# Optimization experiments

Measured on AMD Instinct MI355X. Metric: run time of the kernel, lower is better.

The kernel has to match this reference:

```python
import jax, jax.numpy as jnp
import numpy as np

GRAPH = 50  # top-k neighbors


def setup_inputs() -> dict:
    key = jax.random.key(0)
    k1, k2, k3, k4, k5 = jax.random.split(key, 5)
    B, N, D, C = 2048, 50000, 256, 100
    return {
        "features": jax.random.normal(k1, (B, D), dtype=jnp.float32),
        "anchor_feature": jax.random.normal(k2, (N, D), dtype=jnp.float32),
        "labels": jax.random.randint(k3, (B,), 0, C),
        "t_labels": jax.random.randint(k4, (B,), 0, C),
        "anchor_label": jax.random.randint(k5, (N,), 0, C),
    }


def reference(features, anchor_feature, labels, t_labels, anchor_label):
    # mode == 'knn_sim', reduction=False; t_labels is unpacked but unused.
    # [B, N] dot-product similarity
    sim = jnp.matmul(features, anchor_feature.T)
    # top-k values and indices along anchor dim
    topk_vals, topk_idx = jax.lax.top_k(sim, GRAPH)  # [B, k]
    # label-match mask gathered at the top-k anchors (equivalent to
    # building the full [B, N] eq-mask then torch.gather along dim 1,
    # but gathers anchor labels first to avoid the dense mask)
    nn_labels = anchor_label[topk_idx]               # [B, k]
    mask_k = (labels[:, None] == nn_labels).astype(jnp.float32)
    mean_log_prob_pos = mask_k.sum(axis=1) / GRAPH   # [B]
    mean_sim = topk_vals.sum(axis=1) / GRAPH         # [B]
    # NaN scrub (x != x) -> 0, as in the torch code
    mean_log_prob_pos = jnp.where(jnp.isnan(mean_log_prob_pos), 0.0, mean_log_prob_pos)
    loss = -mean_log_prob_pos                        # [B] (reduction=False)
    return loss, mean_sim
```

## Files before the change

### kernel.cpp

```cpp
#include <hip/hip_runtime.h>
#include <math.h>

#define B_ROWS 2048
#define N_ANCH 50000
#define DIM    256
#define TOPK   50

#define BT 128
#define AT 256
#define KC 32
#define NCHUNK 8
#define NCH 16
#define CHUNK 3125
#define NTILES 13
#define NSAMP 4096
#define CAPG 2048

#define NRB (B_ROWS / BT)
#define TSF (NRB * 8 * 512)
#define TSA (NCH * NTILES * 8 * 1024)

typedef __attribute__((ext_vector_type(8))) short bf16x8;
typedef __attribute__((ext_vector_type(8))) unsigned short u16x8;
typedef __attribute__((ext_vector_type(4))) float f32x4;

#define OFF_B 0
#define OFF_A 16384
#define BUFB  24576
#define SMEM_S (3 * BUFB)
#define SMEM_L (2 * BUFB)

__device__ __forceinline__ void gl_lds16(const void* g, void* l) {
    __builtin_amdgcn_global_load_lds(
        (const __attribute__((address_space(1))) unsigned int*)g,
        (__attribute__((address_space(3))) unsigned int*)l, 16, 0, 0);
}

template<int N>
__device__ __forceinline__ void wait_vmcnt() {
    asm volatile("s_waitcnt vmcnt(%0)" :: "n"(N) : "memory");
}
__device__ __forceinline__ void wait_lgkm0() {
    asm volatile("s_waitcnt lgkmcnt(0)" ::: "memory");
}
__device__ __forceinline__ void pipe_bar() {
    asm volatile("" ::: "memory");
    __builtin_amdgcn_s_barrier();
    asm volatile("" ::: "memory");
}

__device__ __forceinline__ unsigned short f2bf(float x) {
    unsigned u = __float_as_uint(x);
    u += 0x7FFFu + ((u >> 16) & 1u);
    return (unsigned short)(u >> 16);
}

__device__ __forceinline__ unsigned f2ord(float f) {
    unsigned u = __float_as_uint(f);
    return (u & 0x80000000u) ? ~u : (u | 0x80000000u);
}
__device__ __forceinline__ float ord2f(unsigned o) {
    return (o & 0x80000000u) ? __uint_as_float(o & 0x7FFFFFFFu) : __uint_as_float(~o);
}


__global__ __launch_bounds__(256)
void fnorm_feat(const float* __restrict__ x, float* __restrict__ fnorm)
{
    const int lane = threadIdx.x & 63, w = threadIdx.x >> 6;
    const int row  = blockIdx.x * 4 + w;
    float4 v = ((const float4*)(x + (size_t)row * DIM))[lane];
    float s = v.x * v.x + v.y * v.y + v.z * v.z + v.w * v.w;
    #pragma unroll
    for (int off = 32; off; off >>= 1) s += __shfl_down(s, off);
    if (lane == 0) fnorm[row] = sqrtf(s);
}

__global__ __launch_bounds__(256)
void amax_anc(const float* __restrict__ x, int nrows, unsigned* __restrict__ outbits)
{
    __shared__ float wmax[4];
    const int lane = threadIdx.x & 63, w = threadIdx.x >> 6;
    float mx = 0.f;
    for (int i = 0; i < 32; ++i) {
        const int row = blockIdx.x * 128 + w * 32 + i;
        if (row < nrows) {
            float4 v = ((const float4*)(x + (size_t)row * DIM))[lane];
            float s = v.x * v.x + v.y * v.y + v.z * v.z + v.w * v.w;
            #pragma unroll
            for (int off = 32; off; off >>= 1) s += __shfl_down(s, off);
            mx = fmaxf(mx, s);
        }
    }
    if (lane == 0) wmax[w] = mx;
    __syncthreads();
    if (threadIdx.x == 0) {
        float m = fmaxf(fmaxf(wmax[0], wmax[1]), fmaxf(wmax[2], wmax[3]));
        atomicMax(outbits, __float_as_uint(m));
    }
}

__device__ __forceinline__ u16x8 cvt8h(const float4 v0, const float4 v1) {
    float f[8] = {v0.x, v0.y, v0.z, v0.w, v1.x, v1.y, v1.z, v1.w};
    u16x8 h;
    #pragma unroll
    for (int j = 0; j < 8; ++j) h[j] = f2bf(f[j]);
    return h;
}

__global__ __launch_bounds__(256)
void split_pack_feat(const float* __restrict__ x, unsigned short* __restrict__ hi)
{
    const int S  = blockIdx.x * 256 + threadIdx.x;
    const int s  = S & 511;
    const int c  = (S >> 9) & 7;
    const int rb = S >> 12;
    const int r  = s & 127;
    const int kq = s >> 7;
    const int row = (rb << 7) + r;
    const int k   = (c << 5) + (kq << 3);
    const float4* src = (const float4*)(x + (size_t)row * DIM + k);
    *(u16x8*)(hi + (size_t)S * 8) = cvt8h(src[0], src[1]);
}

__global__ __launch_bounds__(256)
void split_pack_anc(const float* __restrict__ x, unsigned short* __restrict__ hi)
{
    const int S    = blockIdx.x * 256 + threadIdx.x;
    const int s    = S & 1023;
    const int c    = (S >> 10) & 7;
    const int tg   = S >> 13;
    const int cidx = tg / NTILES;
    const int tile = tg - cidx * NTILES;
    int a = cidx * CHUNK + (tile << 8) + (s & 255);
    if (a >= N_ANCH) a = N_ANCH - 1;
    const int k = (c << 5) + ((s >> 8) << 3);
    const float4* src = (const float4*)(x + (size_t)a * DIM + k);
    *(u16x8*)(hi + (size_t)S * 8) = cvt8h(src[0], src[1]);
}

#define STAGE_LOADS 3
__device__ __forceinline__ void stage_tile(unsigned char* sb,
                                           const unsigned short* __restrict__ Bsrc,
                                           const unsigned short* __restrict__ Asrc,
                                           int w, int lane)
{
    #pragma unroll
    for (int i = 0; i < 2; ++i) {
        const int t = (w << 1) + i;
        gl_lds16(Bsrc + ((size_t)t << 9) + (lane << 3), sb + OFF_B + (t << 10));
    }
    gl_lds16(Asrc + (((w << 6) + lane) << 3), sb + OFF_A + (w << 10));
}

__device__ __forceinline__ void compute_tile(const unsigned char* sb,
                                             int wm, int wn, int quad, int lx,
                                             f32x4 (&acc)[4][4])
{
    bf16x8 bf[4], af[4];
    #pragma unroll
    for (int tn = 0; tn < 4; ++tn) {
        const int a = (wn << 6) + (tn << 4) + lx;
        bf[tn] = *(const bf16x8*)(sb + OFF_B + (quad << 12) + (a << 4));
    }
    #pragma unroll
    for (int tm = 0; tm < 4; ++tm) {
        const int r = (wm << 6) + (tm << 4) + lx;
        af[tm] = *(const bf16x8*)(sb + OFF_A + (quad << 11) + (r << 4));
    }
    __builtin_amdgcn_s_setprio(1);
    #pragma unroll
    for (int tm = 0; tm < 4; ++tm)
        #pragma unroll
        for (int tn = 0; tn < 4; ++tn)
            acc[tm][tn] = __builtin_amdgcn_mfma_f32_16x16x32_bf16(af[tm], bf[tn], acc[tm][tn], 0, 0, 0);
    __builtin_amdgcn_s_setprio(0);
}

__global__ __launch_bounds__(512, 4)
void knn_sample_gemm(const unsigned short* __restrict__ pfhi,
                     const unsigned short* __restrict__ pahi,
                     float* __restrict__ sims)
{
    __shared__ __align__(16) unsigned char sMem[SMEM_S];

    const int tid  = threadIdx.x;
    const int w    = tid >> 6;
    const int lane = tid & 63;
    const int quad = lane >> 4;
    const int lx   = lane & 15;
    const int wm   = w >> 2;
    const int wn   = w & 3;

    const int id   = blockIdx.x;
    const int xcd  = id & 7;
    const int t    = id >> 3;
    const int rb   = t & 15;
    const int cidx = ((t >> 4) << 3) | xcd;
    const int rbase = rb * BT;
    const int tg    = cidx * NTILES;

    auto bsrc = [&](int c) { return pahi + (((size_t)(tg << 3)) + c) * 8192; };
    auto asrc = [&](int c) { return pfhi + (((size_t)(rb << 3)) + c) * 4096; };

    f32x4 acc[4][4];
    const f32x4 z = {0.f, 0.f, 0.f, 0.f};
    #pragma unroll
    for (int tm = 0; tm < 4; ++tm)
        #pragma unroll
        for (int tn = 0; tn < 4; ++tn) acc[tm][tn] = z;

    stage_tile(sMem + 0 * BUFB, bsrc(0), asrc(0), w, lane);
    stage_tile(sMem + 1 * BUFB, bsrc(1), asrc(1), w, lane);
    __syncthreads();

    for (int it = 0; it < NCHUNK; ++it) {
        if (it + 2 < NCHUNK)
            stage_tile(sMem + ((it + 2) % 3) * BUFB, bsrc(it + 2), asrc(it + 2), w, lane);
        compute_tile(sMem + (it % 3) * BUFB, wm, wn, quad, lx, acc);
        wait_lgkm0();
        if (it + 2 < NCHUNK)      wait_vmcnt<STAGE_LOADS>();
        else if (it + 1 < NCHUNK) wait_vmcnt<0>();
        pipe_bar();
    }

    #pragma unroll
    for (int tm = 0; tm < 4; ++tm)
        #pragma unroll
        for (int tn = 0; tn < 4; ++tn)
            #pragma unroll
            for (int reg = 0; reg < 4; ++reg) {
                int row = rbase + (wm << 6) + (tm << 4) + (quad << 2) + reg;
                int col = (wn << 6) + (tn << 4) + lx;
                sims[(size_t)row * NSAMP + cidx * AT + col] = acc[tm][tn][reg];
            }
}

__global__ __launch_bounds__(256)
void bisect_thresh(const float* __restrict__ sims,
                   uint2* __restrict__ cand, int* __restrict__ cnt,
                   float* __restrict__ Tcut, float* __restrict__ eps2arr,
                   const float* __restrict__ fnorm, const unsigned* __restrict__ amaxb)
{
    __shared__ float sv[NSAMP];
    __shared__ float s_rmin[4], s_rmax[4];
    __shared__ int   s_c, s_ns;

    const int row = blockIdx.x;
    const int tid = threadIdx.x;
    const int lane = tid & 63, w = tid >> 6;
    const unsigned long long below = (lane == 0) ? 0ull : (~0ull >> (64 - lane));

    const float anorm = sqrtf(__uint_as_float(*amaxb));
    const float eps2  = 2.f * (0.004f * fnorm[row] * anorm + 0.1f);

    const float4* S4 = (const float4*)(sims + (size_t)row * NSAMP);
    for (int i = tid; i < NSAMP / 4; i += 256) ((float4*)sv)[i] = S4[i];
    __syncthreads();

    float lmin = INFINITY, lmax = -INFINITY;
    for (int e0 = 0; e0 < NSAMP; e0 += 256) {
        float v = sv[e0 + tid];
        lmin = fminf(lmin, v); lmax = fmaxf(lmax, v);
    }
    #pragma unroll
    for (int off = 32; off; off >>= 1) {
        lmin = fminf(lmin, __shfl_down(lmin, off));
        lmax = fmaxf(lmax, __shfl_down(lmax, off));
    }
    if (lane == 0) { s_rmin[w] = lmin; s_rmax[w] = lmax; }
    __syncthreads();
    float lo = fminf(fminf(s_rmin[0], s_rmin[1]), fminf(s_rmin[2], s_rmin[3]));
    float mx = fmaxf(fmaxf(s_rmax[0], s_rmax[1]), fmaxf(s_rmax[2], s_rmax[3]));
    float hi = ord2f(f2ord(mx) + 1);
    int clo = NSAMP;
    for (int it = 0; it < 32 && clo > 64; ++it) {
        float mid = 0.5f * (lo + hi);
        if (tid == 0) s_c = 0;
        __syncthreads();
        int lc = 0;
        for (int e0 = 0; e0 < NSAMP; e0 += 256) lc += (sv[e0 + tid] >= mid);
        #pragma unroll
        for (int off = 32; off; off >>= 1) lc += __shfl_down(lc, off);
        if (lane == 0) atomicAdd(&s_c, lc);
        __syncthreads();
        int c = s_c;
        if (c >= TOPK) { lo = mid; clo = c; } else hi = mid;
        __syncthreads();
    }
    const float cut = lo - eps2;
    if (tid == 0) { Tcut[row] = cut; eps2arr[row] = eps2; s_ns = 0; }
    __syncthreads();

    for (int e0 = 0; e0 < NSAMP; e0 += 256) {
        int e = e0 + tid;
        float v = sv[e];
        bool pred = (v >= cut);
        unsigned long long mk = __ballot(pred);
        int base = 0;
        if (lane == 0) base = atomicAdd(&s_ns, __popcll(mk));
        base = __shfl(base, 0);
        if (pred) {
            int ofs = base + __popcll(mk & below);
            int anchor = (e >> 8) * CHUNK + (e & 255);
            if (ofs < CAPG)
                cand[(size_t)row * CAPG + ofs] = make_uint2(__float_as_uint(v), (unsigned)anchor);
        }
    }
    __syncthreads();
    if (tid == 0) cnt[row] = s_ns;
}

__global__ __launch_bounds__(512, 4)
void knn_mfma_append(const unsigned short* __restrict__ pfhi,
                     const unsigned short* __restrict__ pahi,
                     const float* __restrict__ Tcut,
                     uint2* __restrict__ cand, int* __restrict__ cnt)
{
    __shared__ __align__(16) unsigned char sMem[SMEM_L];
    __shared__ float s_T[BT];

    const int tid  = threadIdx.x;
    const int w    = tid >> 6;
    const int lane = tid & 63;
    const int quad = lane >> 4;
    const int lx   = lane & 15;
    const int wm   = w >> 2;
    const int wn   = w & 3;

    const int id   = blockIdx.x;
    const int xcd  = id & 7;
    const int t    = id >> 3;
    const int rb   = t & 15;
    const int gseq = t >> 4;
    const int g    = (gseq << 3) | xcd;
    const int cidx = g & 15;
    const int tile = 1 + (g >> 4);
    const int rbase = rb * BT;

    if (tid < BT) s_T[tid] = Tcut[rbase + tid];

    auto bsrc = [&](int c) {
        return pahi + (((size_t)((cidx * NTILES + tile) << 3)) + c) * 8192;
    };
    auto asrc = [&](int c) { return pfhi + (((size_t)(rb << 3)) + c) * 4096; };

    stage_tile(sMem, bsrc(0), asrc(0), w, lane);
    __syncthreads();

    float thr[4][4];
    #pragma unroll
    for (int tm = 0; tm < 4; ++tm)
        #pragma unroll
        for (int reg = 0; reg < 4; ++reg)
            thr[tm][reg] = s_T[(wm << 6) + (tm << 4) + (quad << 2) + reg];

    f32x4 acc[4][4];
    const f32x4 z = {0.f, 0.f, 0.f, 0.f};
    #pragma unroll
    for (int tm = 0; tm < 4; ++tm)
        #pragma unroll
        for (int tn = 0; tn < 4; ++tn) acc[tm][tn] = z;

    int cur = 0;
    for (int c = 0; c < NCHUNK; ++c) {
        if (c + 1 < NCHUNK) {
            stage_tile(sMem + (cur ^ 1) * BUFB, bsrc(c + 1), asrc(c + 1), w, lane);
            wait_vmcnt<STAGE_LOADS>();
        } else {
            wait_vmcnt<0>();
        }
        pipe_bar();
        compute_tile(sMem + cur * BUFB, wm, wn, quad, lx, acc);
        wait_lgkm0();
        pipe_bar();
        cur ^= 1;
    }

    const int abase = cidx * CHUNK + tile * AT;
    const int valid = min(AT, CHUNK - tile * AT);

    #pragma unroll
    for (int tm = 0; tm < 4; ++tm)
        #pragma unroll
        for (int tn = 0; tn < 4; ++tn)
            #pragma unroll
            for (int reg = 0; reg < 4; ++reg) {
                const float v    = acc[tm][tn][reg];
                const int   aoff = (wn << 6) + (tn << 4) + lx;
                if (aoff < valid && v >= thr[tm][reg]) {
                    const int row = rbase + (wm << 6) + (tm << 4) + (quad << 2) + reg;
                    int slot = atomicAdd(&cnt[row], 1);
                    if (slot < CAPG)
                        cand[(size_t)row * CAPG + slot] =
                            make_uint2(__float_as_uint(v), (unsigned)(abase + aoff));
                }
            }
}

__device__ __forceinline__ float coop_dot3(const float4 f4,
                                           const float* __restrict__ anc,
                                           int id, int lane)
{
    float4 a4 = ((const float4*)(anc + (size_t)id * DIM))[lane];
    float av[4] = {a4.x, a4.y, a4.z, a4.w};
    float fw[4] = {f4.x, f4.y, f4.z, f4.w};
    float s = 0.f;
    #pragma unroll
    for (int e = 0; e < 4; ++e) {
        float a = av[e], f = fw[e];
        float ah = __uint_as_float((unsigned)f2bf(a) << 16);
        float al = __uint_as_float((unsigned)f2bf(a - ah) << 16);
        float fh = __uint_as_float((unsigned)f2bf(f) << 16);
        float fl = __uint_as_float((unsigned)f2bf(f - fh) << 16);
        s += fh * ah + fl * ah + fh * al;
    }
    #pragma unroll
    for (int off = 32; off; off >>= 1) s += __shfl_down(s, off);
    return s;
}

__global__ __launch_bounds__(256)
void knn_final(const uint2* __restrict__ cand, const int* __restrict__ cnt,
               const int* __restrict__ labels, const int* __restrict__ anchor_label,
               const float* __restrict__ feat, const float* __restrict__ anc,
               const float* __restrict__ eps2arr, float* __restrict__ out)
{
    __shared__ float pv[CAPG];
    __shared__ int   pi[CAPG];
    __shared__ float fv[CAPG];
    __shared__ int   fi[CAPG];
    __shared__ float s_rmin[4], s_rmax[4];
    __shared__ int   s_c, s_m, s_cm;
    __shared__ float s_sum;

    const int row = blockIdx.x;
    const int tid = threadIdx.x;
    const int lane = tid & 63, w = tid >> 6;
    const unsigned long long below = (lane == 0) ? 0ull : (~0ull >> (64 - lane));
    const float eps2 = eps2arr[row];

    if (tid == 0) { s_sum = 0.f; s_cm = 0; }

    const float4 f4 = ((const float4*)(feat + (size_t)row * DIM))[lane];

    int ns = cnt[row]; if (ns > CAPG) ns = CAPG;
    for (int e0 = 0; e0 < ns; e0 += 256) {
        int e = e0 + tid;
        if (e < ns) {
            uint2 c = cand[(size_t)row * CAPG + e];
            pv[e] = __uint_as_float(c.x); pi[e] = (int)c.y;
        }
    }
    __syncthreads();
    const int mylab = labels[row];

    float lmin = INFINITY, lmax = -INFINITY;
    for (int e0 = 0; e0 < ns; e0 += 256) {
        int e = e0 + tid;
        if (e < ns) { float v = pv[e]; lmin = fminf(lmin, v); lmax = fmaxf(lmax, v); }
    }
    #pragma unroll
    for (int off = 32; off; off >>= 1) {
        lmin = fminf(lmin, __shfl_down(lmin, off));
        lmax = fmaxf(lmax, __shfl_down(lmax, off));
    }
    if (lane == 0) { s_rmin[w] = lmin; s_rmax[w] = lmax; }
    __syncthreads();
    float lo = fminf(fminf(s_rmin[0], s_rmin[1]), fminf(s_rmin[2], s_rmin[3]));
    float mx = fmaxf(fmaxf(s_rmax[0], s_rmax[1]), fmaxf(s_rmax[2], s_rmax[3]));
    float hi = ord2f(f2ord(mx) + 1);
    int clo = ns;
    for (int it = 0; it < 32 && clo > 64; ++it) {
        float mid = 0.5f * (lo + hi);
        if (tid == 0) s_c = 0;
        __syncthreads();
        int lc = 0;
        for (int e0 = 0; e0 < ns; e0 += 256) {
            int e = e0 + tid;
            lc += (e < ns && pv[e] >= mid);
        }
        #pragma unroll
        for (int off = 32; off; off >>= 1) lc += __shfl_down(lc, off);
        if (lane == 0) atomicAdd(&s_c, lc);
        __syncthreads();
        int c = s_c;
        if (c >= TOPK) { lo = mid; clo = c; } else hi = mid;
        __syncthreads();
    }

    if (tid == 0) s_m = 0;
    __syncthreads();
    const float cut = lo - eps2;
    for (int e0 = 0; e0 < ns; e0 += 256) {
        int e = e0 + tid;
        bool pred = (e < ns) && (pv[e] >= cut);
        unsigned long long mk = __ballot(pred);
        int base = 0;
        if (lane == 0) base = atomicAdd(&s_m, __popcll(mk));
        base = __shfl(base, 0);
        if (pred) {
            int ofs = base + __popcll(mk & below);
            if (ofs < CAPG) { fv[ofs] = pv[e]; fi[ofs] = pi[e]; }
        }
    }
    __syncthreads();
    int m = s_m; if (m > CAPG) m = CAPG;

    for (int j = w; j < m; j += 4) {
        float v = coop_dot3(f4, anc, fi[j], lane);
        if (lane == 0) fv[j] = v;
    }
    __syncthreads();

    lmin = INFINITY; lmax = -INFINITY;
    for (int e0 = 0; e0 < m; e0 += 256) {
        int e = e0 + tid;
        if (e < m) { float v = fv[e]; lmin = fminf(lmin, v); lmax = fmaxf(lmax, v); }
    }
    #pragma unroll
    for (int off = 32; off; off >>= 1) {
        lmin = fminf(lmin, __shfl_down(lmin, off));
        lmax = fmaxf(lmax, __shfl_down(lmax, off));
    }
    if (lane == 0) { s_rmin[w] = lmin; s_rmax[w] = lmax; }
    __syncthreads();
    float lo2 = fminf(fminf(s_rmin[0], s_rmin[1]), fminf(s_rmin[2], s_rmin[3]));
    float mx2 = fmaxf(fmaxf(s_rmax[0], s_rmax[1]), fmaxf(s_rmax[2], s_rmax[3]));
    float hi2 = ord2f(f2ord(mx2) + 1);
    int clo2 = m;
    for (int it = 0; it < 32 && clo2 > 96; ++it) {
        float mid = 0.5f * (lo2 + hi2);
        if (tid == 0) s_c = 0;
        __syncthreads();
        int lc = 0;
        for (int e0 = 0; e0 < m; e0 += 256) {
            int e = e0 + tid;
            lc += (e < m && fv[e] >= mid);
        }
        #pragma unroll
        for (int off = 32; off; off >>= 1) lc += __shfl_down(lc, off);
        if (lane == 0) atomicAdd(&s_c, lc);
        __syncthreads();
        int c = s_c;
        if (c >= TOPK) { lo2 = mid; clo2 = c; } else hi2 = mid;
        __syncthreads();
    }

    for (int e = tid; e < m; e += 256) {
        float v = fv[e];
        if (v >= lo2) {
            int idx = fi[e];
            int r = 0;
            for (int q = 0; q < m; ++q) {
                float vq = fv[q];
                r += (vq > v) || (vq == v && fi[q] < idx);
            }
            if (r < TOPK) {
                atomicAdd(&s_sum, v);
                if (anchor_label[idx] == mylab) atomicAdd(&s_cm, 1);
            }
        }
    }
    __syncthreads();
    if (tid == 0) {
        float mlp = (float)s_cm / (float)TOPK;
        out[row]          = -mlp;
        out[B_ROWS + row] = s_sum / (float)TOPK;
    }
}

extern "C" void kernel_launch(void* const* d_in, const int* in_sizes, int n_in,
                              void* d_out, int out_size, void* d_ws, size_t ws_size,
                              hipStream_t stream)
{
    const float* feat         = (const float*)d_in[0];
    const float* anc          = (const float*)d_in[1];
    const int*   labels       = (const int*)d_in[2];
    const int*   anchor_label = (const int*)d_in[4];
    float* out = (float*)d_out;

    char* ws = (char*)d_ws;
    size_t off = 0;
    unsigned short* pfhi = (unsigned short*)(ws + off); off += (size_t)TSF * 16;
    unsigned short* pahi = (unsigned short*)(ws + off); off += (size_t)TSA * 16;
    float* sims = (float*)(ws + off);        off += (size_t)B_ROWS * NSAMP * 4;
    uint2* cand = (uint2*)sims;
    int*   cnt     = (int*)(ws + off);       off += (size_t)B_ROWS * 4;
    float* Tcut    = (float*)(ws + off);     off += (size_t)B_ROWS * 4;
    float* eps2arr = (float*)(ws + off);     off += (size_t)B_ROWS * 4;
    float* fnorm   = (float*)(ws + off);     off += (size_t)B_ROWS * 4;
    unsigned* amaxb = (unsigned*)(ws + off); off += 16;

    hipMemsetAsync(amaxb, 0, 4, stream);
    hipLaunchKernelGGL(fnorm_feat, dim3(B_ROWS / 4), dim3(256), 0, stream,
                       feat, fnorm);
    hipLaunchKernelGGL(amax_anc, dim3((N_ANCH + 127) / 128), dim3(256), 0, stream,
                       anc, N_ANCH, amaxb);
    hipLaunchKernelGGL(split_pack_feat, dim3(TSF / 256), dim3(256), 0, stream,
                       feat, pfhi);
    hipLaunchKernelGGL(split_pack_anc, dim3(TSA / 256), dim3(256), 0, stream,
                       anc, pahi);
    hipLaunchKernelGGL(knn_sample_gemm, dim3(256), dim3(512), 0, stream,
                       pfhi, pahi, sims);
    hipLaunchKernelGGL(bisect_thresh, dim3(B_ROWS), dim3(256), 0, stream,
                       sims, cand, cnt, Tcut, eps2arr, fnorm, amaxb);
    hipLaunchKernelGGL(knn_mfma_append, dim3(3072), dim3(512), 0, stream,
                       pfhi, pahi, Tcut, cand, cnt);
    hipLaunchKernelGGL(knn_final, dim3(B_ROWS), dim3(256), 0, stream,
                       cand, cnt, labels, anchor_label, feat, anc, eps2arr, out);
}
```

Baseline: 554.6 us.

## Load GEMM operands directly from global memory instead of staging through LDS

Both MFMA GEMM kernels drop the shared-memory multi-buffered staging pipeline, with its global_load_lds copies, waitcnts and barriers. Each wave now reads its bf16 fragments straight from the pre-packed global layout into registers. The aim is to remove barrier and LDS overhead, relying on L2/cache reuse of the shared A/B tiles across waves. The cost is more global/L2 traffic, since the 4 waves sharing a tile each reload it, and no explicit prefetch overlap.

```diff
diff --git a/kernel.cpp b/kernel.cpp
--- a/kernel.cpp
+++ b/kernel.cpp
@@ -23,31 +23,6 @@
 typedef __attribute__((ext_vector_type(8))) short bf16x8;
 typedef __attribute__((ext_vector_type(8))) unsigned short u16x8;
 typedef __attribute__((ext_vector_type(4))) float f32x4;
-
-#define OFF_B 0
-#define OFF_A 16384
-#define BUFB  24576
-#define SMEM_S (3 * BUFB)
-#define SMEM_L (2 * BUFB)
-
-__device__ __forceinline__ void gl_lds16(const void* g, void* l) {
-    __builtin_amdgcn_global_load_lds(
-        (const __attribute__((address_space(1))) unsigned int*)g,
-        (__attribute__((address_space(3))) unsigned int*)l, 16, 0, 0);
-}
-
-template<int N>
-__device__ __forceinline__ void wait_vmcnt() {
-    asm volatile("s_waitcnt vmcnt(%0)" :: "n"(N) : "memory");
-}
-__device__ __forceinline__ void wait_lgkm0() {
-    asm volatile("s_waitcnt lgkmcnt(0)" ::: "memory");
-}
-__device__ __forceinline__ void pipe_bar() {
-    asm volatile("" ::: "memory");
-    __builtin_amdgcn_s_barrier();
-    asm volatile("" ::: "memory");
-}
 
 __device__ __forceinline__ unsigned short f2bf(float x) {
     unsigned u = __float_as_uint(x);
@@ -139,42 +114,31 @@
     *(u16x8*)(hi + (size_t)S * 8) = cvt8h(src[0], src[1]);
 }
 
-#define STAGE_LOADS 3
-__device__ __forceinline__ void stage_tile(unsigned char* sb,
-                                           const unsigned short* __restrict__ Bsrc,
-                                           const unsigned short* __restrict__ Asrc,
-                                           int w, int lane)
-{
-    #pragma unroll
-    for (int i = 0; i < 2; ++i) {
-        const int t = (w << 1) + i;
-        gl_lds16(Bsrc + ((size_t)t << 9) + (lane << 3), sb + OFF_B + (t << 10));
-    }
-    gl_lds16(Asrc + (((w << 6) + lane) << 3), sb + OFF_A + (w << 10));
-}
-
-__device__ __forceinline__ void compute_tile(const unsigned char* sb,
-                                             int wm, int wn, int quad, int lx,
-                                             f32x4 (&acc)[4][4])
-{
-    bf16x8 bf[4], af[4];
-    #pragma unroll
-    for (int tn = 0; tn < 4; ++tn) {
-        const int a = (wn << 6) + (tn << 4) + lx;
-        bf[tn] = *(const bf16x8*)(sb + OFF_B + (quad << 12) + (a << 4));
-    }
-    #pragma unroll
-    for (int tm = 0; tm < 4; ++tm) {
-        const int r = (wm << 6) + (tm << 4) + lx;
-        af[tm] = *(const bf16x8*)(sb + OFF_A + (quad << 11) + (r << 4));
-    }
-    __builtin_amdgcn_s_setprio(1);
-    #pragma unroll
-    for (int tm = 0; tm < 4; ++tm)
-        #pragma unroll
-        for (int tn = 0; tn < 4; ++tn)
-            acc[tm][tn] = __builtin_amdgcn_mfma_f32_16x16x32_bf16(af[tm], bf[tn], acc[tm][tn], 0, 0, 0);
-    __builtin_amdgcn_s_setprio(0);
+
+__device__ __forceinline__ void gemm_direct(const unsigned short* __restrict__ Abase,
+                                            const unsigned short* __restrict__ Bbase,
+                                            int lane, int wm, int wn,
+                                            f32x4 (&acc)[4][4])
+{
+    const int lx = lane & 15;
+    const int kq = lane >> 4;
+    const unsigned short* Ap = Abase + (kq << 10) + (((wm << 6) + lx) << 3);
+    const unsigned short* Bp = Bbase + (kq << 11) + (((wn << 6) + lx) << 3);
+
+    for (int c = 0; c < NCHUNK; ++c) {
+        const unsigned short* Ac = Ap + (size_t)c * 4096;
+        const unsigned short* Bc = Bp + (size_t)c * 8192;
+        bf16x8 af[4], bf[4];
+        #pragma unroll
+        for (int t = 0; t < 4; ++t) af[t] = *(const bf16x8*)(Ac + (t << 7));
+        #pragma unroll
+        for (int t = 0; t < 4; ++t) bf[t] = *(const bf16x8*)(Bc + (t << 7));
+        #pragma unroll
+        for (int tm = 0; tm < 4; ++tm)
+            #pragma unroll
+            for (int tn = 0; tn < 4; ++tn)
+                acc[tm][tn] = __builtin_amdgcn_mfma_f32_16x16x32_bf16(af[tm], bf[tn], acc[tm][tn], 0, 0, 0);
+    }
 }
 
 __global__ __launch_bounds__(512, 4)
@@ -182,8 +146,6 @@
                      const unsigned short* __restrict__ pahi,
                      float* __restrict__ sims)
 {
-    __shared__ __align__(16) unsigned char sMem[SMEM_S];
-
     const int tid  = threadIdx.x;
     const int w    = tid >> 6;
     const int lane = tid & 63;
@@ -200,8 +162,8 @@
     const int rbase = rb * BT;
     const int tg    = cidx * NTILES;
 
-    auto bsrc = [&](int c) { return pahi + (((size_t)(tg << 3)) + c) * 8192; };
-    auto asrc = [&](int c) { return pfhi + (((size_t)(rb << 3)) + c) * 4096; };
+    const unsigned short* Abase = pfhi + ((size_t)(rb << 3)) * 4096;
+    const unsigned short* Bbase = pahi + ((size_t)(tg << 3)) * 8192;
 
     f32x4 acc[4][4];
     const f32x4 z = {0.f, 0.f, 0.f, 0.f};
@@ -210,19 +172,7 @@
         #pragma unroll
         for (int tn = 0; tn < 4; ++tn) acc[tm][tn] = z;
 
-    stage_tile(sMem + 0 * BUFB, bsrc(0), asrc(0), w, lane);
-    stage_tile(sMem + 1 * BUFB, bsrc(1), asrc(1), w, lane);
-    __syncthreads();
-
-    for (int it = 0; it < NCHUNK; ++it) {
-        if (it + 2 < NCHUNK)
-            stage_tile(sMem + ((it + 2) % 3) * BUFB, bsrc(it + 2), asrc(it + 2), w, lane);
-        compute_tile(sMem + (it % 3) * BUFB, wm, wn, quad, lx, acc);
-        wait_lgkm0();
-        if (it + 2 < NCHUNK)      wait_vmcnt<STAGE_LOADS>();
-        else if (it + 1 < NCHUNK) wait_vmcnt<0>();
-        pipe_bar();
-    }
+    gemm_direct(Abase, Bbase, lane, wm, wn, acc);
 
     #pragma unroll
     for (int tm = 0; tm < 4; ++tm)
@@ -317,9 +267,6 @@
                      const float* __restrict__ Tcut,
                      uint2* __restrict__ cand, int* __restrict__ cnt)
 {
-    __shared__ __align__(16) unsigned char sMem[SMEM_L];
-    __shared__ float s_T[BT];
-
     const int tid  = threadIdx.x;
     const int w    = tid >> 6;
     const int lane = tid & 63;
@@ -338,22 +285,8 @@
     const int tile = 1 + (g >> 4);
     const int rbase = rb * BT;
 
-    if (tid < BT) s_T[tid] = Tcut[rbase + tid];
-
-    auto bsrc = [&](int c) {
-        return pahi + (((size_t)((cidx * NTILES + tile) << 3)) + c) * 8192;
-    };
-    auto asrc = [&](int c) { return pfhi + (((size_t)(rb << 3)) + c) * 4096; };
-
-    stage_tile(sMem, bsrc(0), asrc(0), w, lane);
-    __syncthreads();
-
-    float thr[4][4];
-    #pragma unroll
-    for (int tm = 0; tm < 4; ++tm)
-        #pragma unroll
-        for (int reg = 0; reg < 4; ++reg)
-            thr[tm][reg] = s_T[(wm << 6) + (tm << 4) + (quad << 2) + reg];
+    const unsigned short* Abase = pfhi + ((size_t)(rb << 3)) * 4096;
+    const unsigned short* Bbase = pahi + ((size_t)((cidx * NTILES + tile) << 3)) * 8192;
 
     f32x4 acc[4][4];
     const f32x4 z = {0.f, 0.f, 0.f, 0.f};
@@ -362,20 +295,14 @@
         #pragma unroll
         for (int tn = 0; tn < 4; ++tn) acc[tm][tn] = z;
 
-    int cur = 0;
-    for (int c = 0; c < NCHUNK; ++c) {
-        if (c + 1 < NCHUNK) {
-            stage_tile(sMem + (cur ^ 1) * BUFB, bsrc(c + 1), asrc(c + 1), w, lane);
-            wait_vmcnt<STAGE_LOADS>();
-        } else {
-            wait_vmcnt<0>();
-        }
-        pipe_bar();
-        compute_tile(sMem + cur * BUFB, wm, wn, quad, lx, acc);
-        wait_lgkm0();
-        pipe_bar();
-        cur ^= 1;
-    }
+    gemm_direct(Abase, Bbase, lane, wm, wn, acc);
+
+    float thr[4][4];
+    #pragma unroll
+    for (int tm = 0; tm < 4; ++tm)
+        #pragma unroll
+        for (int reg = 0; reg < 4; ++reg)
+            thr[tm][reg] = Tcut[rbase + (wm << 6) + (tm << 4) + (quad << 2) + reg];
 
     const int abase = cidx * CHUNK + tile * AT;
     const int valid = min(AT, CHUNK - tile * AT);
```

After: 548.9 us. No clear change (-1.0%).
